# Kernel optimization log

Hardware: AMD Instinct MI355X
Metric: run time of the kernel (lower is better)

The kernel has to match this reference:

```python
import jax, jax.numpy as jnp
import numpy as np

N = 100000   # nodes
E = 640000   # edges
IN = 256     # raw input feature dim
D = 128      # post-MLP node feature dim (fixed in FilterGNN)


def setup_inputs() -> dict:
    key = jax.random.key(0)
    ks = jax.random.split(key, 10)
    x = jax.random.normal(ks[0], (N, IN), jnp.float32)
    alpha = jax.random.uniform(ks[1], (E, 1), jnp.float32)  # edge gate logits in [0,1)
    edge_index = jax.random.randint(ks[2], (2, E), 0, N, dtype=jnp.int32)
    norm = jnp.ones((E,), jnp.float32)  # passed to message in the original but unused
    # MLP `lin`: in_channels -> 512 -> 256 -> 128 (kaiming-normal weights, zero bias)
    def kaiming(k, fan_out, fan_in):
        return jax.random.normal(k, (fan_out, fan_in), jnp.float32) * jnp.sqrt(2.0 / fan_in)
    W1 = kaiming(ks[3], 512, IN); b1 = jnp.zeros((512,), jnp.float32)
    W2 = kaiming(ks[4], 256, 512); b2 = jnp.zeros((256,), jnp.float32)
    W3 = kaiming(ks[5], D, 256);  b3 = jnp.zeros((D,), jnp.float32)
    return {"x": x, "alpha": alpha, "edge_index": edge_index, "norm": norm,
            "W1": W1, "b1": b1, "W2": W2, "b2": b2, "W3": W3, "b3": b3}


def reference(x, alpha, edge_index, norm, W1, b1, W2, b2, W3, b3):
    # FilterGNN.lin: Linear-Tanh-Linear-Tanh-Linear  -> [N, 128]
    h = jnp.tanh(x @ W1.T + b1)
    h = jnp.tanh(h @ W2.T + b2)
    h = h @ W3.T + b3
    # FilterGraphConv1: gather x_j, elementwise relu gate, scatter-mean over targets.
    # (The [-1, H, C] view with H*C = 128 is a pure reshape; the gate broadcasts
    #  over all features, so the math is identical without the head split.)
    src, dst = edge_index[0], edge_index[1]
    gate = 2.0 * jax.nn.relu(jax.lax.stop_gradient(alpha) - 0.5)  # [E, 1]
    msg = h[src] * gate                                           # [E, 128] gather + gate
    sums = jax.ops.segment_sum(msg, dst, num_segments=N)          # [N, 128]
    cnt = jax.ops.segment_sum(jnp.ones((E,), h.dtype), dst, num_segments=N)
    out = sums / jnp.maximum(cnt, 1.0)[:, None]                   # scatter-mean (0 if no edges)
    return out
```

## Files before the change

### kernel.cpp

```cpp
#include <hip/hip_runtime.h>

typedef __attribute__((ext_vector_type(8))) short short8;
typedef __attribute__((ext_vector_type(4))) float f32x4;

__device__ __forceinline__ unsigned short f2bf(float f) {
    union { float f; unsigned u; } v; v.f = f;
    unsigned r = v.u + 0x7FFFu + ((v.u >> 16) & 1u);
    return (unsigned short)(r >> 16);
}
__device__ __forceinline__ float bf2f(unsigned short h) {
    union { unsigned u; float f; } v; v.u = ((unsigned)h) << 16;
    return v.f;
}

__device__ __forceinline__ float tanh_fast(float x) {
    float xc = fminf(fmaxf(x, -9.0f), 9.0f);
    float t  = __expf(2.0f * xc);
    return (t - 1.0f) * __builtin_amdgcn_rcpf(t + 1.0f);
}

#define GLD16(gptr, lptr)                                                     \
    __builtin_amdgcn_global_load_lds(                                         \
        (const __attribute__((address_space(1))) unsigned int*)(gptr),        \
        (__attribute__((address_space(3))) unsigned int*)(lptr), 16, 0, 0)

__global__ __launch_bounds__(256) void cast_all(
    const float* __restrict__ x,  unsigned short* __restrict__ xbf,
    const float* __restrict__ W1, unsigned short* __restrict__ w1bf,
    const float* __restrict__ W2, unsigned short* __restrict__ w2bf,
    const float* __restrict__ W3, unsigned short* __restrict__ w3bf,
    int xq)
{
    int t = blockIdx.x * 256 + threadIdx.x;
    const float* s; unsigned short* d; int q;
    if (t < xq) { s = x; d = xbf; q = t; }
    else {
        int u = t - xq;
        if (u < 32768)      { s = W1; d = w1bf; q = u; }
        else if (u < 65536) { s = W2; d = w2bf; q = u - 32768; }
        else if (u < 73728) { s = W3; d = w3bf; q = u - 65536; }
        else return;
    }
    int base = q * 4;
    float4 v = *(const float4*)(s + base);
    unsigned long long p =
        (unsigned long long)f2bf(v.x)
      | ((unsigned long long)f2bf(v.y) << 16)
      | ((unsigned long long)f2bf(v.z) << 32)
      | ((unsigned long long)f2bf(v.w) << 48);
    *(unsigned long long*)(d + base) = p;
}

#define TM 128
#define TN 128
#define BK 64

__global__ __launch_bounds__(256) void gemm_bt(
    const unsigned short* __restrict__ A, const unsigned short* __restrict__ B,
    const float* __restrict__ bias, unsigned short* __restrict__ C,
    int M, int N, int K)
{
    __shared__ __align__(16) short As[TM][BK];
    __shared__ __align__(16) short Bs[TM][BK];

    const int tid  = threadIdx.x;
    const int wave = tid >> 6;
    const int lane = tid & 63;
    const int m0 = blockIdx.x * TM;
    const int n0 = blockIdx.y * TN;
    const int wm = (wave >> 1) * 64;
    const int wn = (wave & 1) * 64;
    const int lm = lane & 15;
    const int quad = lane >> 4;

    const int srow = lane >> 3;
    const int scol = ((lane & 7) ^ srow) * 8;
    const int cc0 = (quad ^ (lm & 7)) * 8;
    const int cc1 = ((4 + quad) ^ (lm & 7)) * 8;

    f32x4 acc[4][4] = {};

    for (int k0 = 0; k0 < K; k0 += BK) {
        #pragma unroll
        for (int i = 0; i < 4; ++i) {
            int row = wave * 32 + i * 8;
            int gr = m0 + row + srow; if (gr >= M) gr = M - 1;
            GLD16(A + (size_t)gr * K + k0 + scol, &As[row][0]);
            GLD16(B + (size_t)(n0 + row + srow) * K + k0 + scol, &Bs[row][0]);
        }
        __syncthreads();

        #pragma unroll
        for (int ks = 0; ks < BK; ks += 32) {
            const int cc = (ks == 0) ? cc0 : cc1;
            short8 af[4], bf_[4];
            #pragma unroll
            for (int i = 0; i < 4; ++i) {
                af[i]  = *(const short8*)&As[wm + i * 16 + lm][cc];
                bf_[i] = *(const short8*)&Bs[wn + i * 16 + lm][cc];
            }
            #pragma unroll
            for (int im = 0; im < 4; ++im)
                #pragma unroll
                for (int in = 0; in < 4; ++in)
                    acc[im][in] = __builtin_amdgcn_mfma_f32_16x16x32_bf16(
                        af[im], bf_[in], acc[im][in], 0, 0, 0);
        }
        __syncthreads();
    }

    #pragma unroll
    for (int im = 0; im < 4; ++im) {
        int gm_base = m0 + wm + im * 16 + quad * 4;
        #pragma unroll
        for (int in = 0; in < 4; ++in) {
            int gn = n0 + wn + in * 16 + lm;
            float bv = bias[gn];
            #pragma unroll
            for (int r = 0; r < 4; ++r) {
                int gm = gm_base + r;
                if (gm < M) {
                    float v = tanh_fast(acc[im][in][r] + bv);
                    C[(size_t)gm * N + gn] = f2bf(v);
                }
            }
        }
    }
}

__global__ __launch_bounds__(256) void gemm23(
    const unsigned short* __restrict__ h1, const unsigned short* __restrict__ W2,
    const float* __restrict__ b2, const unsigned short* __restrict__ W3,
    const float* __restrict__ b3, unsigned short* __restrict__ hout, int M)
{
    __shared__ __align__(16) short As[64][64];
    __shared__ __align__(16) short Bs[256][64];
    __shared__ __align__(16) short h2s[64][264];

    const int tid  = threadIdx.x;
    const int wave = tid >> 6;
    const int lane = tid & 63;
    const int m0 = blockIdx.x * 64;
    const int wm = (wave >> 1) * 32;
    const int lm = lane & 15;
    const int quad = lane >> 4;
    const int srow = lane >> 3;
    const int scol = ((lane & 7) ^ srow) * 8;
    const int cc0 = (quad ^ (lm & 7)) * 8;
    const int cc1 = ((4 + quad) ^ (lm & 7)) * 8;

    {
        const int wn = (wave & 1) * 128;
        f32x4 acc[2][8] = {};
        for (int k0 = 0; k0 < 512; k0 += 64) {
            #pragma unroll
            for (int i = 0; i < 2; ++i) {
                int r0 = wave * 16 + i * 8;
                int gr = m0 + r0 + srow; if (gr >= M) gr = M - 1;
                GLD16(h1 + (size_t)gr * 512 + k0 + scol, &As[r0][0]);
            }
            #pragma unroll
            for (int i = 0; i < 8; ++i) {
                int r0 = wave * 64 + i * 8;
                GLD16(W2 + (size_t)(r0 + srow) * 512 + k0 + scol, &Bs[r0][0]);
            }
            __syncthreads();
            #pragma unroll
            for (int ks = 0; ks < 64; ks += 32) {
                const int cc = (ks == 0) ? cc0 : cc1;
                short8 af[2], bf_[8];
                #pragma unroll
                for (int i = 0; i < 2; ++i) af[i]  = *(const short8*)&As[wm + i * 16 + lm][cc];
                #pragma unroll
                for (int i = 0; i < 8; ++i) bf_[i] = *(const short8*)&Bs[wn + i * 16 + lm][cc];
                #pragma unroll
                for (int im = 0; im < 2; ++im)
                    #pragma unroll
                    for (int in = 0; in < 8; ++in)
                        acc[im][in] = __builtin_amdgcn_mfma_f32_16x16x32_bf16(
                            af[im], bf_[in], acc[im][in], 0, 0, 0);
            }
            __syncthreads();
        }
        #pragma unroll
        for (int im = 0; im < 2; ++im) {
            int rb = wm + im * 16 + quad * 4;
            #pragma unroll
            for (int in = 0; in < 8; ++in) {
                int col = wn + in * 16 + lm;
                float bv = b2[col];
                #pragma unroll
                for (int r = 0; r < 4; ++r)
                    h2s[rb + r][col] = (short)f2bf(tanh_fast(acc[im][in][r] + bv));
            }
        }
    }
    __syncthreads();

    {
        const int wn = (wave & 1) * 64;
        short (*Bs3)[64] = (short(*)[64])&Bs[0][0];
        f32x4 acc[2][4] = {};
        for (int k0 = 0; k0 < 256; k0 += 64) {
            #pragma unroll
            for (int i = 0; i < 4; ++i) {
                int r0 = wave * 32 + i * 8;
                GLD16(W3 + (size_t)(r0 + srow) * 256 + k0 + scol, &Bs3[r0][0]);
            }
            __syncthreads();
            #pragma unroll
            for (int ks = 0; ks < 64; ks += 32) {
                const int cc = (ks == 0) ? cc0 : cc1;
                short8 af[2], bf_[4];
                #pragma unroll
                for (int i = 0; i < 2; ++i)
                    af[i] = *(const short8*)&h2s[wm + i * 16 + lm][k0 + ks + quad * 8];
                #pragma unroll
                for (int i = 0; i < 4; ++i)
                    bf_[i] = *(const short8*)&Bs3[wn + i * 16 + lm][cc];
                #pragma unroll
                for (int im = 0; im < 2; ++im)
                    #pragma unroll
                    for (int in = 0; in < 4; ++in)
                        acc[im][in] = __builtin_amdgcn_mfma_f32_16x16x32_bf16(
                            af[im], bf_[in], acc[im][in], 0, 0, 0);
            }
            __syncthreads();
        }
        #pragma unroll
        for (int im = 0; im < 2; ++im) {
            int gm_base = m0 + wm + im * 16 + quad * 4;
            #pragma unroll
            for (int in = 0; in < 4; ++in) {
                int gn = wn + in * 16 + lm;
                float bv = b3[gn];
                #pragma unroll
                for (int r = 0; r < 4; ++r) {
                    int gm = gm_base + r;
                    if (gm < M)
                        hout[(size_t)gm * 128 + gn] = f2bf(acc[im][in][r] + bv);
                }
            }
        }
    }
}

__global__ __launch_bounds__(256) void edge_hist(
    const int* __restrict__ ei, const float* __restrict__ alpha,
    unsigned long long* __restrict__ deg, int E)
{
    int e = blockIdx.x * 256 + threadIdx.x;
    if (e >= E) return;
    int dst = ei[E + e];
    float gate = 2.0f * fmaxf(alpha[e] - 0.5f, 0.0f);
    atomicAdd(&deg[dst], 0x100000000ULL | (gate > 0.0f ? 1ULL : 0ULL));
}

__global__ __launch_bounds__(256) void scan1(
    const unsigned long long* __restrict__ deg, int* __restrict__ rowptr,
    int* __restrict__ cursor, int* __restrict__ partials, int N)
{
    __shared__ int sums[256];
    int base = blockIdx.x * 1024 + threadIdx.x * 4;
    int v[4];
    #pragma unroll
    for (int i = 0; i < 4; ++i) {
        int idx = base + i;
        v[i] = (idx < N) ? (int)(deg[idx] & 0xffffffffULL) : 0;
    }
    int s = v[0] + v[1] + v[2] + v[3];
    sums[threadIdx.x] = s;
    __syncthreads();
    for (int off = 1; off < 256; off <<= 1) {
        int t = (threadIdx.x >= off) ? sums[threadIdx.x - off] : 0;
        __syncthreads();
        sums[threadIdx.x] += t;
        __syncthreads();
    }
    int excl = sums[threadIdx.x] - s;
    if (threadIdx.x == 255) partials[blockIdx.x] = sums[255];
    int run = excl;
    #pragma unroll
    for (int i = 0; i < 4; ++i) {
        int idx = base + i;
        if (idx < N) { rowptr[idx] = run; cursor[idx] = run; }
        run += v[i];
    }
}

__global__ __launch_bounds__(256) void scan2(int* __restrict__ partials, int nb)
{
    __shared__ int s[256];
    int v = (threadIdx.x < nb) ? partials[threadIdx.x] : 0;
    s[threadIdx.x] = v;
    __syncthreads();
    for (int off = 1; off < 256; off <<= 1) {
        int t = (threadIdx.x >= off) ? s[threadIdx.x - off] : 0;
        __syncthreads();
        s[threadIdx.x] += t;
        __syncthreads();
    }
    partials[threadIdx.x] = s[threadIdx.x] - v;
}

__global__ __launch_bounds__(256) void edge_fill(
    const int* __restrict__ ei, const float* __restrict__ alpha,
    int* __restrict__ cursor, const int* __restrict__ partials,
    int2* __restrict__ recs, int E)
{
    int e = blockIdx.x * 256 + threadIdx.x;
    if (e >= E) return;
    float gate = 2.0f * fmaxf(alpha[e] - 0.5f, 0.0f);
    if (gate > 0.0f) {
        int dst = ei[E + e];
        int src = ei[e];
        int pos = atomicAdd(&cursor[dst], 1) + partials[dst >> 10];
        recs[pos] = make_int2(src, __float_as_int(gate));
    }
}

__global__ __launch_bounds__(256) void node_gather(
    const unsigned short* __restrict__ h, const unsigned long long* __restrict__ deg,
    const int* __restrict__ rowptr, const int* __restrict__ partials,
    const int2* __restrict__ recs, float* __restrict__ out, int N)
{
    int wave = threadIdx.x >> 6;
    int lane = threadIdx.x & 63;
    int node = blockIdx.x * 4 + wave;
    if (node >= N) return;
    unsigned long long d = deg[node];
    int dAll  = __builtin_amdgcn_readfirstlane((int)(d >> 32));
    int dG    = __builtin_amdgcn_readfirstlane((int)(d & 0xffffffffULL));
    int start = __builtin_amdgcn_readfirstlane(rowptr[node] + partials[node >> 10]);
    int qw = lane >> 4, ql = lane & 15;
    float a[8] = {};
    for (int j = 0; j < dG; j += 4) {
        int jj = j + qw;
        int idx = start + (jj < dG ? jj : dG - 1);
        int2 rec = recs[idx];
        float gate = (jj < dG) ? __int_as_float(rec.y) : 0.0f;
        uint4 u = *(const uint4*)(h + ((size_t)rec.x << 7) + ql * 8);
        a[0] += bf2f((unsigned short)(u.x & 0xffffu)) * gate;
        a[1] += bf2f((unsigned short)(u.x >> 16)) * gate;
        a[2] += bf2f((unsigned short)(u.y & 0xffffu)) * gate;
        a[3] += bf2f((unsigned short)(u.y >> 16)) * gate;
        a[4] += bf2f((unsigned short)(u.z & 0xffffu)) * gate;
        a[5] += bf2f((unsigned short)(u.z >> 16)) * gate;
        a[6] += bf2f((unsigned short)(u.w & 0xffffu)) * gate;
        a[7] += bf2f((unsigned short)(u.w >> 16)) * gate;
    }
    #pragma unroll
    for (int i = 0; i < 8; ++i) {
        a[i] += __shfl_xor(a[i], 16);
        a[i] += __shfl_xor(a[i], 32);
    }
    if (qw == 0) {
        float inv = 1.0f / fmaxf((float)dAll, 1.0f);
        float* op = out + ((size_t)node << 7) + ql * 8;
        *(float4*)(op)     = make_float4(a[0] * inv, a[1] * inv, a[2] * inv, a[3] * inv);
        *(float4*)(op + 4) = make_float4(a[4] * inv, a[5] * inv, a[6] * inv, a[7] * inv);
    }
}

extern "C" void kernel_launch(void* const* d_in, const int* in_sizes, int n_in,
                              void* d_out, int out_size, void* d_ws, size_t ws_size,
                              hipStream_t stream) {
    const float* x     = (const float*)d_in[0];
    const float* alpha = (const float*)d_in[1];
    const int*   ei    = (const int*)d_in[2];
    const float* W1 = (const float*)d_in[4];
    const float* b1 = (const float*)d_in[5];
    const float* W2 = (const float*)d_in[6];
    const float* b2 = (const float*)d_in[7];
    const float* W3 = (const float*)d_in[8];
    const float* b3 = (const float*)d_in[9];
    float* out = (float*)d_out;

    const int N = in_sizes[0] / 256;
    const int E = in_sizes[1];
    const int IN = 256, H1 = 512, D = 128;

    char* ws = (char*)d_ws;
    size_t off = 0;
    auto take = [&](size_t bytes) { char* p = ws + off; off = (off + bytes + 255) & ~(size_t)255; return p; };
    unsigned short* xbf  = (unsigned short*)take((size_t)N * IN * 2);
    unsigned short* h1bf = (unsigned short*)take((size_t)N * H1 * 2);
    unsigned short* hbf  = (unsigned short*)take((size_t)N * D  * 2);
    unsigned short* w1bf = (unsigned short*)take((size_t)H1 * IN * 2);
    unsigned short* w2bf = (unsigned short*)take((size_t)256 * H1 * 2);
    unsigned short* w3bf = (unsigned short*)take((size_t)D * 256 * 2);

    char* cbase = (char*)h1bf;
    size_t coff = 0;
    auto ctake = [&](size_t bytes) { char* p = cbase + coff; coff = (coff + bytes + 255) & ~(size_t)255; return p; };
    unsigned long long* deg = (unsigned long long*)ctake((size_t)N * 8);
    int*  rowptr   = (int*)ctake((size_t)N * 4);
    int*  cursor   = (int*)ctake((size_t)N * 4);
    int*  partials = (int*)ctake(256 * 4);
    int2* recs     = (int2*)ctake((size_t)E * 8);

    dim3 blk(256);

    const int xq = N * IN / 4;
    const int castN = xq + 73728;
    cast_all<<<(castN + 255) / 256, blk, 0, stream>>>(x, xbf, W1, w1bf, W2, w2bf, W3, w3bf, xq);

    const int mblk = (N + TM - 1) / TM;
    gemm_bt<<<dim3(mblk, H1 / TN), blk, 0, stream>>>(xbf, w1bf, b1, h1bf, N, H1, IN);
    gemm23<<<(N + 63) / 64, blk, 0, stream>>>(h1bf, w2bf, b2, w3bf, b3, hbf, N);

    hipMemsetAsync(deg, 0, (size_t)N * 8, stream);
    edge_hist<<<(E + 255) / 256, blk, 0, stream>>>(ei, alpha, deg, E);
    const int nb1 = (N + 1023) / 1024;
    scan1<<<nb1, blk, 0, stream>>>(deg, rowptr, cursor, partials, N);
    scan2<<<1, blk, 0, stream>>>(partials, nb1);
    edge_fill<<<(E + 255) / 256, blk, 0, stream>>>(ei, alpha, cursor, partials, recs, E);

    node_gather<<<(N + 3) / 4, blk, 0, stream>>>(hbf, deg, rowptr, partials, recs, out, N);
}
```

Baseline: 408.8 us.

## Fuse all three MLP layers into one kernel with in-kernel x conversion

Replaces the separate x-cast, layer-1 GEMM and layer-2/3 kernels with one 512-thread kernel. It converts x rows to bf16 directly into shared memory and keeps h1 (64x512) in LDS, so the bf16 x copy and the h1 intermediate never go through global memory. The cost is a large LDS footprint (about 131 KB per block), which limits occupancy. W1 is now re-streamed by every 64-row block instead of being amortised over 128-row tiles.

```diff
diff --git a/kernel.cpp b/kernel.cpp
--- a/kernel.cpp
+++ b/kernel.cpp
@@ -19,227 +19,170 @@
     return (t - 1.0f) * __builtin_amdgcn_rcpf(t + 1.0f);
 }
 
+__device__ __forceinline__ unsigned long long pack4(float4 v) {
+    return (unsigned long long)f2bf(v.x)
+         | ((unsigned long long)f2bf(v.y) << 16)
+         | ((unsigned long long)f2bf(v.z) << 32)
+         | ((unsigned long long)f2bf(v.w) << 48);
+}
+
 #define GLD16(gptr, lptr)                                                     \
     __builtin_amdgcn_global_load_lds(                                         \
         (const __attribute__((address_space(1))) unsigned int*)(gptr),        \
         (__attribute__((address_space(3))) unsigned int*)(lptr), 16, 0, 0)
 
-__global__ __launch_bounds__(256) void cast_all(
-    const float* __restrict__ x,  unsigned short* __restrict__ xbf,
+__global__ __launch_bounds__(256) void cast_w(
     const float* __restrict__ W1, unsigned short* __restrict__ w1bf,
     const float* __restrict__ W2, unsigned short* __restrict__ w2bf,
-    const float* __restrict__ W3, unsigned short* __restrict__ w3bf,
-    int xq)
+    const float* __restrict__ W3, unsigned short* __restrict__ w3bf)
 {
     int t = blockIdx.x * 256 + threadIdx.x;
     const float* s; unsigned short* d; int q;
-    if (t < xq) { s = x; d = xbf; q = t; }
-    else {
-        int u = t - xq;
-        if (u < 32768)      { s = W1; d = w1bf; q = u; }
-        else if (u < 65536) { s = W2; d = w2bf; q = u - 32768; }
-        else if (u < 73728) { s = W3; d = w3bf; q = u - 65536; }
-        else return;
-    }
+    if (t < 32768)      { s = W1; d = w1bf; q = t; }
+    else if (t < 65536) { s = W2; d = w2bf; q = t - 32768; }
+    else if (t < 73728) { s = W3; d = w3bf; q = t - 65536; }
+    else return;
     int base = q * 4;
     float4 v = *(const float4*)(s + base);
-    unsigned long long p =
-        (unsigned long long)f2bf(v.x)
-      | ((unsigned long long)f2bf(v.y) << 16)
-      | ((unsigned long long)f2bf(v.z) << 32)
-      | ((unsigned long long)f2bf(v.w) << 48);
-    *(unsigned long long*)(d + base) = p;
-}
-
-#define TM 128
-#define TN 128
-#define BK 64
-
-__global__ __launch_bounds__(256) void gemm_bt(
-    const unsigned short* __restrict__ A, const unsigned short* __restrict__ B,
-    const float* __restrict__ bias, unsigned short* __restrict__ C,
-    int M, int N, int K)
-{
-    __shared__ __align__(16) short As[TM][BK];
-    __shared__ __align__(16) short Bs[TM][BK];
+    *(unsigned long long*)(d + base) = pack4(v);
+}
+
+__global__ __launch_bounds__(512, 2) void mlp_fused(
+    const float* __restrict__ x,
+    const unsigned short* __restrict__ W1, const float* __restrict__ b1,
+    const unsigned short* __restrict__ W2, const float* __restrict__ b2,
+    const unsigned short* __restrict__ W3, const float* __restrict__ b3,
+    unsigned short* __restrict__ hout, int M)
+{
+    __shared__ __align__(16) short Bs[256][64];
+    __shared__ __align__(16) short h1s[64][520];
+    __shared__ __align__(16) short pool[64 * 264];
 
     const int tid  = threadIdx.x;
     const int wave = tid >> 6;
     const int lane = tid & 63;
-    const int m0 = blockIdx.x * TM;
-    const int n0 = blockIdx.y * TN;
-    const int wm = (wave >> 1) * 64;
-    const int wn = (wave & 1) * 64;
-    const int lm = lane & 15;
-    const int quad = lane >> 4;
-
-    const int srow = lane >> 3;
-    const int scol = ((lane & 7) ^ srow) * 8;
-    const int cc0 = (quad ^ (lm & 7)) * 8;
-    const int cc1 = ((4 + quad) ^ (lm & 7)) * 8;
-
-    f32x4 acc[4][4] = {};
-
-    for (int k0 = 0; k0 < K; k0 += BK) {
-        #pragma unroll
-        for (int i = 0; i < 4; ++i) {
-            int row = wave * 32 + i * 8;
-            int gr = m0 + row + srow; if (gr >= M) gr = M - 1;
-            GLD16(A + (size_t)gr * K + k0 + scol, &As[row][0]);
-            GLD16(B + (size_t)(n0 + row + srow) * K + k0 + scol, &Bs[row][0]);
-        }
-        __syncthreads();
-
-        #pragma unroll
-        for (int ks = 0; ks < BK; ks += 32) {
-            const int cc = (ks == 0) ? cc0 : cc1;
-            short8 af[4], bf_[4];
-            #pragma unroll
-            for (int i = 0; i < 4; ++i) {
-                af[i]  = *(const short8*)&As[wm + i * 16 + lm][cc];
-                bf_[i] = *(const short8*)&Bs[wn + i * 16 + lm][cc];
-            }
-            #pragma unroll
-            for (int im = 0; im < 4; ++im)
-                #pragma unroll
-                for (int in = 0; in < 4; ++in)
-                    acc[im][in] = __builtin_amdgcn_mfma_f32_16x16x32_bf16(
-                        af[im], bf_[in], acc[im][in], 0, 0, 0);
-        }
-        __syncthreads();
-    }
-
-    #pragma unroll
-    for (int im = 0; im < 4; ++im) {
-        int gm_base = m0 + wm + im * 16 + quad * 4;
-        #pragma unroll
-        for (int in = 0; in < 4; ++in) {
-            int gn = n0 + wn + in * 16 + lm;
-            float bv = bias[gn];
-            #pragma unroll
-            for (int r = 0; r < 4; ++r) {
-                int gm = gm_base + r;
-                if (gm < M) {
-                    float v = tanh_fast(acc[im][in][r] + bv);
-                    C[(size_t)gm * N + gn] = f2bf(v);
-                }
-            }
-        }
-    }
-}
-
-__global__ __launch_bounds__(256) void gemm23(
-    const unsigned short* __restrict__ h1, const unsigned short* __restrict__ W2,
-    const float* __restrict__ b2, const unsigned short* __restrict__ W3,
-    const float* __restrict__ b3, unsigned short* __restrict__ hout, int M)
-{
-    __shared__ __align__(16) short As[64][64];
-    __shared__ __align__(16) short Bs[256][64];
-    __shared__ __align__(16) short h2s[64][264];
-
-    const int tid  = threadIdx.x;
-    const int wave = tid >> 6;
-    const int lane = tid & 63;
-    const int m0 = blockIdx.x * 64;
-    const int wm = (wave >> 1) * 32;
-    const int lm = lane & 15;
+    const int m0   = blockIdx.x * 64;
+    const int wm   = (wave >> 1) * 16;
+    const int half = wave & 1;
+    const int lm   = lane & 15;
     const int quad = lane >> 4;
     const int srow = lane >> 3;
     const int scol = ((lane & 7) ^ srow) * 8;
-    const int cc0 = (quad ^ (lm & 7)) * 8;
-    const int cc1 = ((4 + quad) ^ (lm & 7)) * 8;
+    const int cc0  = (quad ^ (lm & 7)) * 8;
+    const int cc1  = ((4 + quad) ^ (lm & 7)) * 8;
+
+    short (*xs)[64]   = (short(*)[64])pool;
+    short (*h2s)[264] = (short(*)[264])pool;
 
     {
-        const int wn = (wave & 1) * 128;
-        f32x4 acc[2][8] = {};
+        int gr = m0 + wave * 8 + srow; if (gr >= M) gr = M - 1;
+        const float* xr = x + (size_t)gr * 256;
+        #pragma unroll
+        for (int kt = 0; kt < 4; ++kt) {
+            float4 va = *(const float4*)(xr + kt * 64 + scol);
+            float4 vb = *(const float4*)(xr + kt * 64 + scol + 4);
+            unsigned long long* dp =
+                (unsigned long long*)&xs[kt * 64 + wave * 8 + srow][(lane & 7) * 8];
+            dp[0] = pack4(va); dp[1] = pack4(vb);
+        }
+    }
+
+    for (int nh = 0; nh < 2; ++nh) {
+        f32x4 acc[8] = {};
+        for (int kt = 0; kt < 4; ++kt) {
+            #pragma unroll
+            for (int i = 0; i < 4; ++i) {
+                int r0 = wave * 32 + i * 8;
+                GLD16(W1 + (size_t)(nh * 256 + r0 + srow) * 256 + kt * 64 + scol, &Bs[r0][0]);
+            }
+            __syncthreads();
+            #pragma unroll
+            for (int ks = 0; ks < 2; ++ks) {
+                const int cc = ks ? cc1 : cc0;
+                short8 af = *(const short8*)&xs[kt * 64 + wm + lm][cc];
+                #pragma unroll
+                for (int in = 0; in < 8; ++in) {
+                    short8 bv = *(const short8*)&Bs[half * 128 + in * 16 + lm][cc];
+                    acc[in] = __builtin_amdgcn_mfma_f32_16x16x32_bf16(af, bv, acc[in], 0, 0, 0);
+                }
+            }
+            __syncthreads();
+        }
+        int rb = wm + quad * 4;
+        #pragma unroll
+        for (int in = 0; in < 8; ++in) {
+            int col = nh * 256 + half * 128 + in * 16 + lm;
+            float bv = b1[col];
+            #pragma unroll
+            for (int r = 0; r < 4; ++r)
+                h1s[rb + r][col] = (short)f2bf(tanh_fast(acc[in][r] + bv));
+        }
+    }
+    __syncthreads();
+
+    {
+        f32x4 acc[8] = {};
         for (int k0 = 0; k0 < 512; k0 += 64) {
+            #pragma unroll
+            for (int i = 0; i < 4; ++i) {
+                int r0 = wave * 32 + i * 8;
+                GLD16(W2 + (size_t)(r0 + srow) * 512 + k0 + scol, &Bs[r0][0]);
+            }
+            __syncthreads();
+            #pragma unroll
+            for (int ks = 0; ks < 2; ++ks) {
+                const int cc = ks ? cc1 : cc0;
+                short8 af = *(const short8*)&h1s[wm + lm][k0 + ks * 32 + quad * 8];
+                #pragma unroll
+                for (int in = 0; in < 8; ++in) {
+                    short8 bv = *(const short8*)&Bs[half * 128 + in * 16 + lm][cc];
+                    acc[in] = __builtin_amdgcn_mfma_f32_16x16x32_bf16(af, bv, acc[in], 0, 0, 0);
+                }
+            }
+            __syncthreads();
+        }
+        int rb = wm + quad * 4;
+        #pragma unroll
+        for (int in = 0; in < 8; ++in) {
+            int col = half * 128 + in * 16 + lm;
+            float bv = b2[col];
+            #pragma unroll
+            for (int r = 0; r < 4; ++r)
+                h2s[rb + r][col] = (short)f2bf(tanh_fast(acc[in][r] + bv));
+        }
+    }
+
+    {
+        f32x4 acc[4] = {};
+        for (int k0 = 0; k0 < 256; k0 += 64) {
             #pragma unroll
             for (int i = 0; i < 2; ++i) {
                 int r0 = wave * 16 + i * 8;
-                int gr = m0 + r0 + srow; if (gr >= M) gr = M - 1;
-                GLD16(h1 + (size_t)gr * 512 + k0 + scol, &As[r0][0]);
-            }
-            #pragma unroll
-            for (int i = 0; i < 8; ++i) {
-                int r0 = wave * 64 + i * 8;
-                GLD16(W2 + (size_t)(r0 + srow) * 512 + k0 + scol, &Bs[r0][0]);
-            }
-            __syncthreads();
-            #pragma unroll
-            for (int ks = 0; ks < 64; ks += 32) {
-                const int cc = (ks == 0) ? cc0 : cc1;
-                short8 af[2], bf_[8];
+                GLD16(W3 + (size_t)(r0 + srow) * 256 + k0 + scol, &Bs[r0][0]);
+            }
+            __syncthreads();
+            #pragma unroll
+            for (int ks = 0; ks < 2; ++ks) {
+                const int cc = ks ? cc1 : cc0;
+                short8 af = *(const short8*)&h2s[wm + lm][k0 + ks * 32 + quad * 8];
                 #pragma unroll
-                for (int i = 0; i < 2; ++i) af[i]  = *(const short8*)&As[wm + i * 16 + lm][cc];
-                #pragma unroll
-                for (int i = 0; i < 8; ++i) bf_[i] = *(const short8*)&Bs[wn + i * 16 + lm][cc];
-                #pragma unroll
-                for (int im = 0; im < 2; ++im)
-                    #pragma unroll
-                    for (int in = 0; in < 8; ++in)
-                        acc[im][in] = __builtin_amdgcn_mfma_f32_16x16x32_bf16(
-                            af[im], bf_[in], acc[im][in], 0, 0, 0);
-            }
-            __syncthreads();
-        }
+                for (int in = 0; in < 4; ++in) {
+                    short8 bv = *(const short8*)&Bs[half * 64 + in * 16 + lm][cc];
+                    acc[in] = __builtin_amdgcn_mfma_f32_16x16x32_bf16(af, bv, acc[in], 0, 0, 0);
+                }
+            }
+            __syncthreads();
+        }
+        int gm_base = m0 + wm + quad * 4;
         #pragma unroll
-        for (int im = 0; im < 2; ++im) {
-            int rb = wm + im * 16 + quad * 4;
-            #pragma unroll
-            for (int in = 0; in < 8; ++in) {
-                int col = wn + in * 16 + lm;
-                float bv = b2[col];
-                #pragma unroll
-                for (int r = 0; r < 4; ++r)
-                    h2s[rb + r][col] = (short)f2bf(tanh_fast(acc[im][in][r] + bv));
-            }
-        }
-    }
-    __syncthreads();
-
-    {
-        const int wn = (wave & 1) * 64;
-        short (*Bs3)[64] = (short(*)[64])&Bs[0][0];
-        f32x4 acc[2][4] = {};
-        for (int k0 = 0; k0 < 256; k0 += 64) {
-            #pragma unroll
-            for (int i = 0; i < 4; ++i) {
-                int r0 = wave * 32 + i * 8;
-                GLD16(W3 + (size_t)(r0 + srow) * 256 + k0 + scol, &Bs3[r0][0]);
-            }
-            __syncthreads();
-            #pragma unroll
-            for (int ks = 0; ks < 64; ks += 32) {
-                const int cc = (ks == 0) ? cc0 : cc1;
-                short8 af[2], bf_[4];
-                #pragma unroll
-                for (int i = 0; i < 2; ++i)
-                    af[i] = *(const short8*)&h2s[wm + i * 16 + lm][k0 + ks + quad * 8];
-                #pragma unroll
-                for (int i = 0; i < 4; ++i)
-                    bf_[i] = *(const short8*)&Bs3[wn + i * 16 + lm][cc];
-                #pragma unroll
-                for (int im = 0; im < 2; ++im)
-                    #pragma unroll
-                    for (int in = 0; in < 4; ++in)
-                        acc[im][in] = __builtin_amdgcn_mfma_f32_16x16x32_bf16(
-                            af[im], bf_[in], acc[im][in], 0, 0, 0);
-            }
-            __syncthreads();
-        }
-        #pragma unroll
-        for (int im = 0; im < 2; ++im) {
-            int gm_base = m0 + wm + im * 16 + quad * 4;
-            #pragma unroll
-            for (int in = 0; in < 4; ++in) {
-                int gn = wn + in * 16 + lm;
-                float bv = b3[gn];
-                #pragma unroll
-                for (int r = 0; r < 4; ++r) {
-                    int gm = gm_base + r;
-                    if (gm < M)
-                        hout[(size_t)gm * 128 + gn] = f2bf(acc[im][in][r] + bv);
-                }
+        for (int in = 0; in < 4; ++in) {
+            int gn = half * 64 + in * 16 + lm;
+            float bv = b3[gn];
+            #pragma unroll
+            for (int r = 0; r < 4; ++r) {
+                int gm = gm_base + r;
+                if (gm < M)
+                    hout[(size_t)gm * 128 + gn] = f2bf(acc[in][r] + bv);
             }
         }
     }
@@ -378,36 +321,26 @@
 
     const int N = in_sizes[0] / 256;
     const int E = in_sizes[1];
-    const int IN = 256, H1 = 512, D = 128;
+    const int H1 = 512, D = 128;
 
     char* ws = (char*)d_ws;
     size_t off = 0;
     auto take = [&](size_t bytes) { char* p = ws + off; off = (off + bytes + 255) & ~(size_t)255; return p; };
-    unsigned short* xbf  = (unsigned short*)take((size_t)N * IN * 2);
-    unsigned short* h1bf = (unsigned short*)take((size_t)N * H1 * 2);
     unsigned short* hbf  = (unsigned short*)take((size_t)N * D  * 2);
-    unsigned short* w1bf = (unsigned short*)take((size_t)H1 * IN * 2);
+    unsigned short* w1bf = (unsigned short*)take((size_t)H1 * 256 * 2);
     unsigned short* w2bf = (unsigned short*)take((size_t)256 * H1 * 2);
     unsigned short* w3bf = (unsigned short*)take((size_t)D * 256 * 2);
-
-    char* cbase = (char*)h1bf;
-    size_t coff = 0;
-    auto ctake = [&](size_t bytes) { char* p = cbase + coff; coff = (coff + bytes + 255) & ~(size_t)255; return p; };
-    unsigned long long* deg = (unsigned long long*)ctake((size_t)N * 8);
-    int*  rowptr   = (int*)ctake((size_t)N * 4);
-    int*  cursor   = (int*)ctake((size_t)N * 4);
-    int*  partials = (int*)ctake(256 * 4);
-    int2* recs     = (int2*)ctake((size_t)E * 8);
+    unsigned long long* deg = (unsigned long long*)take((size_t)N * 8);
+    int*  rowptr   = (int*)take((size_t)N * 4);
+    int*  cursor   = (int*)take((size_t)N * 4);
+    int*  partials = (int*)take(256 * 4);
+    int2* recs     = (int2*)take((size_t)E * 8);
 
     dim3 blk(256);
 
-    const int xq = N * IN / 4;
-    const int castN = xq + 73728;
-    cast_all<<<(castN + 255) / 256, blk, 0, stream>>>(x, xbf, W1, w1bf, W2, w2bf, W3, w3bf, xq);
-
-    const int mblk = (N + TM - 1) / TM;
-    gemm_bt<<<dim3(mblk, H1 / TN), blk, 0, stream>>>(xbf, w1bf, b1, h1bf, N, H1, IN);
-    gemm23<<<(N + 63) / 64, blk, 0, stream>>>(h1bf, w2bf, b2, w3bf, b3, hbf, N);
+    cast_w<<<288, blk, 0, stream>>>(W1, w1bf, W2, w2bf, W3, w3bf);
+    mlp_fused<<<(N + 63) / 64, dim3(512), 0, stream>>>(
+        x, w1bf, b1, w2bf, b2, w3bf, b3, hbf, N);
 
     hipMemsetAsync(deg, 0, (size_t)N * 8, stream);
     edge_hist<<<(E + 255) / 256, blk, 0, stream>>>(ei, alpha, deg, E);
```

New measurement: 414.7 us. No clear change (+1.5%).

## Fuse fp32-to-bf16 cast of x into first GEMM and stage output through LDS

Applied to the files above, without the earlier changes.

Removes the separate pass that casts the whole input x to bf16. The first GEMM now loads fp32 x directly, converts it in registers and writes a swizzled bf16 tile into LDS, while only the weights are still cast up front. The epilogue writes the tanh output to an LDS tile and then stores it with coalesced 16-byte writes instead of scattered 2-byte stores. The trade-off is that x is now read in fp32 once per N-block (four times) instead of as bf16, and the A-tile load becomes a synchronous register path rather than a direct global-to-LDS copy.

```diff
diff --git a/kernel.cpp b/kernel.cpp
--- a/kernel.cpp
+++ b/kernel.cpp
@@ -19,85 +19,88 @@
     return (t - 1.0f) * __builtin_amdgcn_rcpf(t + 1.0f);
 }
 
+__device__ __forceinline__ unsigned long long pack4(float4 v) {
+    return (unsigned long long)f2bf(v.x)
+         | ((unsigned long long)f2bf(v.y) << 16)
+         | ((unsigned long long)f2bf(v.z) << 32)
+         | ((unsigned long long)f2bf(v.w) << 48);
+}
+
 #define GLD16(gptr, lptr)                                                     \
     __builtin_amdgcn_global_load_lds(                                         \
         (const __attribute__((address_space(1))) unsigned int*)(gptr),        \
         (__attribute__((address_space(3))) unsigned int*)(lptr), 16, 0, 0)
 
-__global__ __launch_bounds__(256) void cast_all(
-    const float* __restrict__ x,  unsigned short* __restrict__ xbf,
+__global__ __launch_bounds__(256) void cast_w(
     const float* __restrict__ W1, unsigned short* __restrict__ w1bf,
     const float* __restrict__ W2, unsigned short* __restrict__ w2bf,
-    const float* __restrict__ W3, unsigned short* __restrict__ w3bf,
-    int xq)
+    const float* __restrict__ W3, unsigned short* __restrict__ w3bf)
 {
     int t = blockIdx.x * 256 + threadIdx.x;
     const float* s; unsigned short* d; int q;
-    if (t < xq) { s = x; d = xbf; q = t; }
-    else {
-        int u = t - xq;
-        if (u < 32768)      { s = W1; d = w1bf; q = u; }
-        else if (u < 65536) { s = W2; d = w2bf; q = u - 32768; }
-        else if (u < 73728) { s = W3; d = w3bf; q = u - 65536; }
-        else return;
-    }
+    if (t < 32768)      { s = W1; d = w1bf; q = t; }
+    else if (t < 65536) { s = W2; d = w2bf; q = t - 32768; }
+    else if (t < 73728) { s = W3; d = w3bf; q = t - 65536; }
+    else return;
     int base = q * 4;
     float4 v = *(const float4*)(s + base);
-    unsigned long long p =
-        (unsigned long long)f2bf(v.x)
-      | ((unsigned long long)f2bf(v.y) << 16)
-      | ((unsigned long long)f2bf(v.z) << 32)
-      | ((unsigned long long)f2bf(v.w) << 48);
-    *(unsigned long long*)(d + base) = p;
-}
-
-#define TM 128
-#define TN 128
-#define BK 64
-
-__global__ __launch_bounds__(256) void gemm_bt(
-    const unsigned short* __restrict__ A, const unsigned short* __restrict__ B,
-    const float* __restrict__ bias, unsigned short* __restrict__ C,
-    int M, int N, int K)
-{
-    __shared__ __align__(16) short As[TM][BK];
-    __shared__ __align__(16) short Bs[TM][BK];
+    *(unsigned long long*)(d + base) = pack4(v);
+}
+
+__global__ __launch_bounds__(256) void gemm1(
+    const float* __restrict__ x, const unsigned short* __restrict__ W1,
+    const float* __restrict__ b1, unsigned short* __restrict__ C, int M)
+{
+    __shared__ __align__(16) short lds[128 * 136];
+    short* As = lds;
+    short* Bs = lds + 128 * 64;
 
     const int tid  = threadIdx.x;
     const int wave = tid >> 6;
     const int lane = tid & 63;
-    const int m0 = blockIdx.x * TM;
-    const int n0 = blockIdx.y * TN;
+    const int m0 = blockIdx.x * 128;
+    const int n0 = blockIdx.y * 128;
     const int wm = (wave >> 1) * 64;
     const int wn = (wave & 1) * 64;
     const int lm = lane & 15;
     const int quad = lane >> 4;
-
     const int srow = lane >> 3;
     const int scol = ((lane & 7) ^ srow) * 8;
     const int cc0 = (quad ^ (lm & 7)) * 8;
     const int cc1 = ((4 + quad) ^ (lm & 7)) * 8;
 
+    const int ac = tid & 7;
+    const int arb = tid >> 3;
+
     f32x4 acc[4][4] = {};
 
-    for (int k0 = 0; k0 < K; k0 += BK) {
+    for (int kt = 0; kt < 4; ++kt) {
+        const int k0 = kt * 64;
+        #pragma unroll
+        for (int j = 0; j < 4; ++j) {
+            int r = arb + j * 32;
+            int gr = m0 + r; if (gr >= M) gr = M - 1;
+            const float* p = x + (size_t)gr * 256 + k0 + ac * 8;
+            float4 a0 = *(const float4*)(p);
+            float4 a1 = *(const float4*)(p + 4);
+            unsigned long long* d =
+                (unsigned long long*)&As[r * 64 + ((ac ^ (r & 7)) * 8)];
+            d[0] = pack4(a0); d[1] = pack4(a1);
+        }
         #pragma unroll
         for (int i = 0; i < 4; ++i) {
-            int row = wave * 32 + i * 8;
-            int gr = m0 + row + srow; if (gr >= M) gr = M - 1;
-            GLD16(A + (size_t)gr * K + k0 + scol, &As[row][0]);
-            GLD16(B + (size_t)(n0 + row + srow) * K + k0 + scol, &Bs[row][0]);
-        }
-        __syncthreads();
-
-        #pragma unroll
-        for (int ks = 0; ks < BK; ks += 32) {
-            const int cc = (ks == 0) ? cc0 : cc1;
+            int r0 = wave * 32 + i * 8;
+            GLD16(W1 + (size_t)(n0 + r0 + srow) * 256 + k0 + scol, &Bs[r0 * 64]);
+        }
+        __syncthreads();
+        #pragma unroll
+        for (int ks = 0; ks < 2; ++ks) {
+            const int cc = ks ? cc1 : cc0;
             short8 af[4], bf_[4];
             #pragma unroll
             for (int i = 0; i < 4; ++i) {
-                af[i]  = *(const short8*)&As[wm + i * 16 + lm][cc];
-                bf_[i] = *(const short8*)&Bs[wn + i * 16 + lm][cc];
+                af[i]  = *(const short8*)&As[(wm + i * 16 + lm) * 64 + cc];
+                bf_[i] = *(const short8*)&Bs[(wn + i * 16 + lm) * 64 + cc];
             }
             #pragma unroll
             for (int im = 0; im < 4; ++im)
@@ -109,21 +112,29 @@
         __syncthreads();
     }
 
+    short* Ct = lds;
     #pragma unroll
-    for (int im = 0; im < 4; ++im) {
-        int gm_base = m0 + wm + im * 16 + quad * 4;
-        #pragma unroll
-        for (int in = 0; in < 4; ++in) {
-            int gn = n0 + wn + in * 16 + lm;
-            float bv = bias[gn];
+    for (int in = 0; in < 4; ++in) {
+        float bb = b1[n0 + wn + in * 16 + lm];
+        int col = wn + in * 16 + lm;
+        #pragma unroll
+        for (int im = 0; im < 4; ++im) {
             #pragma unroll
             for (int r = 0; r < 4; ++r) {
-                int gm = gm_base + r;
-                if (gm < M) {
-                    float v = tanh_fast(acc[im][in][r] + bv);
-                    C[(size_t)gm * N + gn] = f2bf(v);
-                }
-            }
+                int row = wm + im * 16 + quad * 4 + r;
+                Ct[row * 136 + col] = (short)f2bf(tanh_fast(acc[im][in][r] + bb));
+            }
+        }
+    }
+    __syncthreads();
+    #pragma unroll
+    for (int j = 0; j < 8; ++j) {
+        int idx = j * 256 + tid;
+        int row = idx >> 4, ch = idx & 15;
+        int gm = m0 + row;
+        if (gm < M) {
+            uint4 v = *(const uint4*)&Ct[row * 136 + ch * 8];
+            *(uint4*)(C + (size_t)gm * 512 + n0 + ch * 8) = v;
         }
     }
 }
@@ -378,15 +389,14 @@
 
     const int N = in_sizes[0] / 256;
     const int E = in_sizes[1];
-    const int IN = 256, H1 = 512, D = 128;
+    const int H1 = 512, D = 128;
 
     char* ws = (char*)d_ws;
     size_t off = 0;
     auto take = [&](size_t bytes) { char* p = ws + off; off = (off + bytes + 255) & ~(size_t)255; return p; };
-    unsigned short* xbf  = (unsigned short*)take((size_t)N * IN * 2);
     unsigned short* h1bf = (unsigned short*)take((size_t)N * H1 * 2);
     unsigned short* hbf  = (unsigned short*)take((size_t)N * D  * 2);
-    unsigned short* w1bf = (unsigned short*)take((size_t)H1 * IN * 2);
+    unsigned short* w1bf = (unsigned short*)take((size_t)H1 * 256 * 2);
     unsigned short* w2bf = (unsigned short*)take((size_t)256 * H1 * 2);
     unsigned short* w3bf = (unsigned short*)take((size_t)D * 256 * 2);
 
@@ -401,12 +411,9 @@
 
     dim3 blk(256);
 
-    const int xq = N * IN / 4;
-    const int castN = xq + 73728;
-    cast_all<<<(castN + 255) / 256, blk, 0, stream>>>(x, xbf, W1, w1bf, W2, w2bf, W3, w3bf, xq);
-
-    const int mblk = (N + TM - 1) / TM;
-    gemm_bt<<<dim3(mblk, H1 / TN), blk, 0, stream>>>(xbf, w1bf, b1, h1bf, N, H1, IN);
+    cast_w<<<288, blk, 0, stream>>>(W1, w1bf, W2, w2bf, W3, w3bf);
+    const int mblk = (N + 127) / 128;
+    gemm1<<<dim3(mblk, 4), blk, 0, stream>>>(x, w1bf, b1, h1bf, N);
     gemm23<<<(N + 63) / 64, blk, 0, stream>>>(h1bf, w2bf, b2, w3bf, b3, hbf, N);
 
     hipMemsetAsync(deg, 0, (size_t)N * 8, stream);
```

New measurement: 418.8 us. 2.5% more time.

## Fuse edge histogram into second GEMM launch and replace two-pass scan with atomic offsets

Applied to the files above, without the earlier changes.

Appends the edge-degree histogram blocks to the gemm23 grid so the atomics can run alongside the MLP GEMM, which removes one launch. The two-level prefix scan becomes a single pass where each block takes its base offset from a global atomic counter, which drops scan2 and the partials lookups in edge_fill and node_gather. Segments end up in arbitrary block order, but each node's range stays contiguous, so the output is still correct. The scratch buffers move to the xbf region, and a few extra memset bytes cover the counter.

```diff
diff --git a/kernel.cpp b/kernel.cpp
--- a/kernel.cpp
+++ b/kernel.cpp
@@ -128,14 +128,26 @@
     }
 }
 
-__global__ __launch_bounds__(256) void gemm23(
+__global__ __launch_bounds__(256) void gemm23_hist(
     const unsigned short* __restrict__ h1, const unsigned short* __restrict__ W2,
     const float* __restrict__ b2, const unsigned short* __restrict__ W3,
-    const float* __restrict__ b3, unsigned short* __restrict__ hout, int M)
+    const float* __restrict__ b3, unsigned short* __restrict__ hout, int M,
+    const int* __restrict__ ei, const float* __restrict__ alpha,
+    unsigned long long* __restrict__ deg, int E, int gblk)
 {
     __shared__ __align__(16) short As[64][64];
     __shared__ __align__(16) short Bs[256][64];
     __shared__ __align__(16) short h2s[64][264];
+
+    if ((int)blockIdx.x >= gblk) {
+        int e = (blockIdx.x - gblk) * 256 + threadIdx.x;
+        if (e < E) {
+            int dst = ei[E + e];
+            float gate = 2.0f * fmaxf(alpha[e] - 0.5f, 0.0f);
+            atomicAdd(&deg[dst], 0x100000000ULL | (gate > 0.0f ? 1ULL : 0ULL));
+        }
+        return;
+    }
 
     const int tid  = threadIdx.x;
     const int wave = tid >> 6;
@@ -245,22 +257,12 @@
     }
 }
 
-__global__ __launch_bounds__(256) void edge_hist(
-    const int* __restrict__ ei, const float* __restrict__ alpha,
-    unsigned long long* __restrict__ deg, int E)
-{
-    int e = blockIdx.x * 256 + threadIdx.x;
-    if (e >= E) return;
-    int dst = ei[E + e];
-    float gate = 2.0f * fmaxf(alpha[e] - 0.5f, 0.0f);
-    atomicAdd(&deg[dst], 0x100000000ULL | (gate > 0.0f ? 1ULL : 0ULL));
-}
-
 __global__ __launch_bounds__(256) void scan1(
     const unsigned long long* __restrict__ deg, int* __restrict__ rowptr,
-    int* __restrict__ cursor, int* __restrict__ partials, int N)
+    int* __restrict__ cursor, int* __restrict__ gcounter, int N)
 {
     __shared__ int sums[256];
+    __shared__ int base_sh;
     int base = blockIdx.x * 1024 + threadIdx.x * 4;
     int v[4];
     #pragma unroll
@@ -278,8 +280,9 @@
         __syncthreads();
     }
     int excl = sums[threadIdx.x] - s;
-    if (threadIdx.x == 255) partials[blockIdx.x] = sums[255];
-    int run = excl;
+    if (threadIdx.x == 255) base_sh = atomicAdd(gcounter, sums[255]);
+    __syncthreads();
+    int run = base_sh + excl;
     #pragma unroll
     for (int i = 0; i < 4; ++i) {
         int idx = base + i;
@@ -288,25 +291,9 @@
     }
 }
 
-__global__ __launch_bounds__(256) void scan2(int* __restrict__ partials, int nb)
-{
-    __shared__ int s[256];
-    int v = (threadIdx.x < nb) ? partials[threadIdx.x] : 0;
-    s[threadIdx.x] = v;
-    __syncthreads();
-    for (int off = 1; off < 256; off <<= 1) {
-        int t = (threadIdx.x >= off) ? s[threadIdx.x - off] : 0;
-        __syncthreads();
-        s[threadIdx.x] += t;
-        __syncthreads();
-    }
-    partials[threadIdx.x] = s[threadIdx.x] - v;
-}
-
 __global__ __launch_bounds__(256) void edge_fill(
     const int* __restrict__ ei, const float* __restrict__ alpha,
-    int* __restrict__ cursor, const int* __restrict__ partials,
-    int2* __restrict__ recs, int E)
+    int* __restrict__ cursor, int2* __restrict__ recs, int E)
 {
     int e = blockIdx.x * 256 + threadIdx.x;
     if (e >= E) return;
@@ -314,15 +301,15 @@
     if (gate > 0.0f) {
         int dst = ei[E + e];
         int src = ei[e];
-        int pos = atomicAdd(&cursor[dst], 1) + partials[dst >> 10];
+        int pos = atomicAdd(&cursor[dst], 1);
         recs[pos] = make_int2(src, __float_as_int(gate));
     }
 }
 
 __global__ __launch_bounds__(256) void node_gather(
     const unsigned short* __restrict__ h, const unsigned long long* __restrict__ deg,
-    const int* __restrict__ rowptr, const int* __restrict__ partials,
-    const int2* __restrict__ recs, float* __restrict__ out, int N)
+    const int* __restrict__ rowptr, const int2* __restrict__ recs,
+    float* __restrict__ out, int N)
 {
     int wave = threadIdx.x >> 6;
     int lane = threadIdx.x & 63;
@@ -331,7 +318,7 @@
     unsigned long long d = deg[node];
     int dAll  = __builtin_amdgcn_readfirstlane((int)(d >> 32));
     int dG    = __builtin_amdgcn_readfirstlane((int)(d & 0xffffffffULL));
-    int start = __builtin_amdgcn_readfirstlane(rowptr[node] + partials[node >> 10]);
+    int start = __builtin_amdgcn_readfirstlane(rowptr[node]);
     int qw = lane >> 4, ql = lane & 15;
     float a[8] = {};
     for (int j = 0; j < dG; j += 4) {
@@ -390,13 +377,13 @@
     unsigned short* w2bf = (unsigned short*)take((size_t)256 * H1 * 2);
     unsigned short* w3bf = (unsigned short*)take((size_t)D * 256 * 2);
 
-    char* cbase = (char*)h1bf;
+    char* cbase = (char*)xbf;
     size_t coff = 0;
     auto ctake = [&](size_t bytes) { char* p = cbase + coff; coff = (coff + bytes + 255) & ~(size_t)255; return p; };
     unsigned long long* deg = (unsigned long long*)ctake((size_t)N * 8);
+    int*  gcounter = (int*)ctake(256);
     int*  rowptr   = (int*)ctake((size_t)N * 4);
     int*  cursor   = (int*)ctake((size_t)N * 4);
-    int*  partials = (int*)ctake(256 * 4);
     int2* recs     = (int2*)ctake((size_t)E * 8);
 
     dim3 blk(256);
@@ -407,14 +394,16 @@
 
     const int mblk = (N + TM - 1) / TM;
     gemm_bt<<<dim3(mblk, H1 / TN), blk, 0, stream>>>(xbf, w1bf, b1, h1bf, N, H1, IN);
-    gemm23<<<(N + 63) / 64, blk, 0, stream>>>(h1bf, w2bf, b2, w3bf, b3, hbf, N);
-
-    hipMemsetAsync(deg, 0, (size_t)N * 8, stream);
-    edge_hist<<<(E + 255) / 256, blk, 0, stream>>>(ei, alpha, deg, E);
+
+    hipMemsetAsync(deg, 0, (size_t)N * 8 + 256, stream);
+    const int gblk = (N + 63) / 64;
+    const int eblk = (E + 255) / 256;
+    gemm23_hist<<<gblk + eblk, blk, 0, stream>>>(
+        h1bf, w2bf, b2, w3bf, b3, hbf, N, ei, alpha, deg, E, gblk);
+
     const int nb1 = (N + 1023) / 1024;
-    scan1<<<nb1, blk, 0, stream>>>(deg, rowptr, cursor, partials, N);
-    scan2<<<1, blk, 0, stream>>>(partials, nb1);
-    edge_fill<<<(E + 255) / 256, blk, 0, stream>>>(ei, alpha, cursor, partials, recs, E);
-
-    node_gather<<<(N + 3) / 4, blk, 0, stream>>>(hbf, deg, rowptr, partials, recs, out, N);
-}
+    scan1<<<nb1, blk, 0, stream>>>(deg, rowptr, cursor, gcounter, N);
+    edge_fill<<<eblk, blk, 0, stream>>>(ei, alpha, cursor, recs, E);
+
+    node_gather<<<(N + 3) / 4, blk, 0, stream>>>(hbf, deg, rowptr, recs, out, N);
+}
```

Result: faster. 393.4 us (-3.8%).
